# Optimization experiments

Measured on AMD Instinct MI355X. Metric: run time of the kernel, lower is better.

## Reference

```python
import jax, jax.numpy as jnp
import numpy as np

INPUT_DIM = 1024
HIDDEN_DIM = 1024
FORGET_BIAS = 0.0


def setup_inputs() -> dict:
    key = jax.random.key(0)
    ks = jax.random.split(key, 8)
    x = jax.random.normal(ks[0], (1024, 32, INPUT_DIM), dtype=jnp.float32)
    state = jnp.zeros((1, 32, HIDDEN_DIM), dtype=jnp.float32)
    std = 0.1
    wm_z = std * jax.random.normal(ks[1], (HIDDEN_DIM, INPUT_DIM), dtype=jnp.float32)
    wm_f = std * jax.random.normal(ks[2], (HIDDEN_DIM, INPUT_DIM), dtype=jnp.float32)
    wv_z = std * jax.random.normal(ks[3], (1, HIDDEN_DIM), dtype=jnp.float32)
    wv_f = std * jax.random.normal(ks[4], (1, HIDDEN_DIM), dtype=jnp.float32)
    bias_z = std * jax.random.normal(ks[5], (1, HIDDEN_DIM), dtype=jnp.float32)
    bias_f = std * jax.random.normal(ks[6], (1, HIDDEN_DIM), dtype=jnp.float32) + FORGET_BIAS
    return {"x": x, "state": state, "wm_z": wm_z, "wm_f": wm_f,
            "wv_z": wv_z, "wv_f": wv_f, "bias_z": bias_z, "bias_f": bias_f}


def reference(x, state, wm_z, wm_f, wv_z, wv_f, bias_z, bias_f):
    # x: [slen, bsz, in_dim]; state: [1, bsz, hidden]
    hidden_prev = state[0]  # [bsz, hidden]
    # Pre-activation input projections (batched GEMM over all timesteps).
    out_z = jnp.einsum('sbi,hi->sbh', x, wm_z)  # [slen, bsz, hidden]
    out_f = jnp.einsum('sbi,hi->sbh', x, wm_f)

    def step(cell, zf):
        z_, f_ = zf
        z_part = jnp.tanh(z_ + wv_z * cell + bias_z)
        f_part = jax.nn.sigmoid(f_ + wv_f * cell + bias_f)
        new_cell = cell * f_part + (1.0 - f_part) * z_part
        return new_cell, new_cell

    _, new_cells = jax.lax.scan(step, hidden_prev, (out_z, out_f))
    return new_cells  # [slen, bsz, hidden]
```

## Files before the change

kernel.cpp:

```cpp
#include <hip/hip_runtime.h>
#include <hip/hip_fp16.h>

#define S_LEN 1024
#define BSZ   32
#define IN_DIM 1024
#define HID   1024
#define MDIM  (S_LEN*BSZ)
#define NDIM  (2*HID)
#define KDIM  IN_DIM

typedef __attribute__((ext_vector_type(8)))  _Float16 half8;
typedef __attribute__((ext_vector_type(2)))  _Float16 half2v;
typedef __attribute__((ext_vector_type(4)))  float    floatx4;

#define NXV ((MDIM*KDIM)/8)
__global__ void cvt_xw_kernel(const float* __restrict__ x,
                              const float* __restrict__ wz, const float* __restrict__ wf,
                              _Float16* __restrict__ xh, _Float16* __restrict__ wh) {
    int idx = blockIdx.x * blockDim.x + threadIdx.x;
    const float4* s4;
    half8* dst;
    if (idx < NXV) {
        s4 = (const float4*)x + (size_t)idx * 2;
        dst = (half8*)xh + idx;
    } else {
        int wi = idx - NXV;
        int e0 = wi * 8;
        int r   = e0 >> 10;
        int col = e0 & 1023;
        int g = r >> 5, sub = r & 31;
        const float* src = (sub < 16)
            ? wz + ((size_t)(g * 16 + sub)      * KDIM + col)
            : wf + ((size_t)(g * 16 + sub - 16) * KDIM + col);
        s4 = (const float4*)src;
        dst = (half8*)wh + wi;
    }
    float4 a = s4[0], b = s4[1];
    half8 h;
    h[0] = (_Float16)a.x; h[1] = (_Float16)a.y; h[2] = (_Float16)a.z; h[3] = (_Float16)a.w;
    h[4] = (_Float16)b.x; h[5] = (_Float16)b.y; h[6] = (_Float16)b.z; h[7] = (_Float16)b.w;
    *dst = h;
}

#define BM 256
#define BN 256
#define BK 64
#define TPB 4
#define NGT (TPB * 16)
#define NIT (NGT / 2)

__global__ __launch_bounds__(512, 2) void gemm_f16_kernel(
    const _Float16* __restrict__ A, const _Float16* __restrict__ B,
    uint* __restrict__ zf) {
    __shared__ __attribute__((aligned(128))) _Float16 smem[65536];
    char* smb = (char*)smem;

    const int tid  = threadIdx.x;
    const int lane = tid & 63;
    const int wv   = tid >> 6;
    const int wm_off = (wv >> 2) * 128;
    const int wn_off = (wv & 3) * 64;

    const int b      = blockIdx.x;
    const int mchunk = (b & 7) + 8 * ((b >> 3) & 3);
    const int m_bs   = mchunk * (TPB * BM);
    const int n0g    = (b >> 5) * BN;

    const int fr  = lane & 15;
    const int fkb = (lane >> 4) * 16;

    const int srow = lane >> 3;
    const int skb  = ((lane & 7) ^ srow) << 4;

    floatx4 acc[8][4] = {};

    auto STAGE_A = [&](int g, int R0) {
        int kt = g & 15, mt = (g >> 4) & 3;
        int r = R0 + wv * 8 + srow;
        const _Float16* gp = A + (size_t)(m_bs + mt * BM + r) * KDIM + kt * BK + (skb >> 1);
        __builtin_amdgcn_global_load_lds(
            (const __attribute__((address_space(1))) void*)gp,
            (__attribute__((address_space(3))) void*)(smb + (g & 1) * 65536 + (R0 + wv * 8) * 128),
            16, 0, 0);
    };
    auto STAGE_B = [&](int g, int R0) {
        int kt = g & 15;
        int r = R0 + wv * 8 + srow;
        const _Float16* gp = B + (size_t)(n0g + r) * KDIM + kt * BK + (skb >> 1);
        __builtin_amdgcn_global_load_lds(
            (const __attribute__((address_space(1))) void*)gp,
            (__attribute__((address_space(3))) void*)(smb + (g & 1) * 65536 + 32768 + (R0 + wv * 8) * 128),
            16, 0, 0);
    };
    auto LD8 = [&](int rb, int r, int kb) -> half8 {
        return *(const half8*)(smb + rb + r * 128 + (kb ^ ((r & 7) << 4)));
    };

    STAGE_B(0, 0);   STAGE_B(0, 64);
    STAGE_A(0, 0);   STAGE_A(0, 128);
    STAGE_B(0, 128); STAGE_B(0, 192);
    STAGE_A(0, 64);  STAGE_A(0, 192);
    STAGE_B(1, 0);   STAGE_B(1, 64);
    STAGE_A(1, 0);   STAGE_A(1, 128);
    STAGE_B(1, 128); STAGE_B(1, 192);
    asm volatile("s_waitcnt vmcnt(6)" ::: "memory");
    __builtin_amdgcn_s_barrier();
    asm volatile("" ::: "memory");

    half8 bfr[4][2];
    half8 afrA[2][2], afrB[2][2];
    for (int it = 0; it < NIT; ++it) {
        const int  t    = 2 * it;
        const bool more = (it < NIT - 1);
        #pragma unroll
        for (int ph = 0; ph < 8; ++ph) {
            const int q     = ph & 3;
            const int bbase = (ph >> 2) * 65536;

            if (q == 0) {
                #pragma unroll
                for (int j = 0; j < 4; ++j)
                    #pragma unroll
                    for (int ks = 0; ks < 2; ++ks)
                        bfr[j][ks] = LD8(bbase + 32768, wn_off + j * 16 + fr, ks * 64 + fkb);
                #pragma unroll
                for (int ii = 0; ii < 2; ++ii)
                    #pragma unroll
                    for (int ks = 0; ks < 2; ++ks) {
                        afrA[ii][ks] = LD8(bbase, wm_off + ii * 16 + fr,        ks * 64 + fkb);
                        afrB[ii][ks] = LD8(bbase, wm_off + (2 + ii) * 16 + fr,  ks * 64 + fkb);
                    }
            } else if (q == 1) {
                #pragma unroll
                for (int ii = 0; ii < 2; ++ii)
                    #pragma unroll
                    for (int ks = 0; ks < 2; ++ks)
                        afrA[ii][ks] = LD8(bbase, wm_off + (4 + ii) * 16 + fr, ks * 64 + fkb);
            } else if (q == 2) {
                #pragma unroll
                for (int ii = 0; ii < 2; ++ii)
                    #pragma unroll
                    for (int ks = 0; ks < 2; ++ks)
                        afrB[ii][ks] = LD8(bbase, wm_off + (6 + ii) * 16 + fr, ks * 64 + fkb);
            }

            if (ph == 0) {
                STAGE_A(t + 1, 64);  STAGE_A(t + 1, 192);
            } else if (more) {
                if      (ph == 1) { STAGE_B(t + 2, 0);   STAGE_B(t + 2, 64);  }
                else if (ph == 2) { STAGE_A(t + 2, 0);   STAGE_A(t + 2, 128); }
                else if (ph == 3) { STAGE_B(t + 2, 128); STAGE_B(t + 2, 192); }
                else if (ph == 4) { STAGE_A(t + 2, 64);  STAGE_A(t + 2, 192); }
                else if (ph == 5) { STAGE_B(t + 3, 0);   STAGE_B(t + 3, 64);  }
                else if (ph == 6) { STAGE_A(t + 3, 0);   STAGE_A(t + 3, 128); }
                else              { STAGE_B(t + 3, 128); STAGE_B(t + 3, 192); }
            }

            __builtin_amdgcn_s_barrier();
            asm volatile("" ::: "memory");
            __builtin_amdgcn_s_setprio(1);
            if (q == 0 || q == 2) {
                #pragma unroll
                for (int ks = 0; ks < 2; ++ks)
                    #pragma unroll
                    for (int ii = 0; ii < 2; ++ii)
                        #pragma unroll
                        for (int j = 0; j < 4; ++j)
                            acc[2 * q + ii][j] = __builtin_amdgcn_mfma_f32_16x16x32_f16(
                                afrA[ii][ks], bfr[j][ks], acc[2 * q + ii][j], 0, 0, 0);
            } else {
                #pragma unroll
                for (int ks = 0; ks < 2; ++ks)
                    #pragma unroll
                    for (int ii = 0; ii < 2; ++ii)
                        #pragma unroll
                        for (int j = 0; j < 4; ++j)
                            acc[2 * q + ii][j] = __builtin_amdgcn_mfma_f32_16x16x32_f16(
                                afrB[ii][ks], bfr[j][ks], acc[2 * q + ii][j], 0, 0, 0);
            }
            __builtin_amdgcn_s_setprio(0);
            if (ph == 3) {
                if (more) asm volatile("s_waitcnt vmcnt(6)" ::: "memory");
                else      asm volatile("s_waitcnt vmcnt(0)" ::: "memory");
            } else if (ph == 7) {
                if (more) asm volatile("s_waitcnt vmcnt(6)" ::: "memory");
            }
            __builtin_amdgcn_s_barrier();
            asm volatile("" ::: "memory");
        }

        if ((it & 7) == 7) {
            const int m0   = m_bs + (it >> 3) * BM;
            const int orow = (lane >> 4) * 4;
            const int ocol = lane & 15;
            const int gb   = (n0g + wn_off) >> 5;
            #pragma unroll
            for (int i = 0; i < 8; ++i)
                #pragma unroll
                for (int p2 = 0; p2 < 2; ++p2) {
                    int hh = (gb + p2) * 16 + ocol;
                    #pragma unroll
                    for (int r = 0; r < 4; ++r) {
                        int row = m0 + wm_off + i * 16 + orow + r;
                        half2v v;
                        v[0] = (_Float16)acc[i][2 * p2][r];
                        v[1] = (_Float16)acc[i][2 * p2 + 1][r];
                        *(half2v*)(zf + (size_t)row * HID + hh) = v;
                    }
                }
            #pragma unroll
            for (int i = 0; i < 8; ++i)
                #pragma unroll
                for (int j = 0; j < 4; ++j)
                    acc[i][j] = (floatx4)0.0f;
        }
    }
}

#define UNR 32
__device__ __forceinline__ float fast_exp2(float x) {
    float r;
    asm("v_exp_f32 %0, %1" : "=v"(r) : "v"(x));
    return r;
}
__global__ __launch_bounds__(64) void scan_kernel(
    const uint* __restrict__ zf, float* __restrict__ out,
    const float* __restrict__ state,
    const float* __restrict__ wvz, const float* __restrict__ wvf,
    const float* __restrict__ bz, const float* __restrict__ bfv) {
    const int t = blockIdx.x * 64 + threadIdx.x;
    const int h = t & (HID - 1);
    const int stride = BSZ * HID;

    float cell = state[t];
    const float L2E = 1.44269504088896f;
    const float azt = 2.0f * L2E * wvz[h];
    const float czt = 2.0f * L2E * bz[h];
    const float aft = -L2E * wvf[h];
    const float cft = -L2E * bfv[h];

    const uint* p = zf + t;
    float* po = out + t;

    uint buf[UNR];
    #pragma unroll
    for (int u = 0; u < UNR; ++u) buf[u] = p[(size_t)u * stride];

    for (int s0 = 0; s0 < S_LEN; s0 += UNR) {
        uint nb[UNR];
        if (s0 + UNR < S_LEN) {
            #pragma unroll
            for (int u = 0; u < UNR; ++u)
                nb[u] = p[(size_t)(s0 + UNR + u) * stride];
        }
        #pragma unroll
        for (int u = 0; u < UNR; ++u) {
            half2v h2 = __builtin_bit_cast(half2v, buf[u]);
            float zb = fmaf((float)h2[0], 2.0f * L2E, czt);
            float fb = fmaf((float)h2[1], -L2E, cft);
            float ez = fast_exp2(fmaf(azt, cell, zb));
            float zp = fmaf(-2.0f, __builtin_amdgcn_rcpf(ez + 1.0f), 1.0f);
            float ef = fast_exp2(fmaf(aft, cell, fb));
            float fp = __builtin_amdgcn_rcpf(ef + 1.0f);
            cell = fmaf(cell - zp, fp, zp);
            po[(size_t)(s0 + u) * stride] = cell;
        }
        #pragma unroll
        for (int u = 0; u < UNR; ++u) buf[u] = nb[u];
    }
}

extern "C" void kernel_launch(void* const* d_in, const int* in_sizes, int n_in,
                              void* d_out, int out_size, void* d_ws, size_t ws_size,
                              hipStream_t stream) {
    const float* x      = (const float*)d_in[0];
    const float* state  = (const float*)d_in[1];
    const float* wm_z   = (const float*)d_in[2];
    const float* wm_f   = (const float*)d_in[3];
    const float* wv_z   = (const float*)d_in[4];
    const float* wv_f   = (const float*)d_in[5];
    const float* bias_z = (const float*)d_in[6];
    const float* bias_f = (const float*)d_in[7];
    float* out = (float*)d_out;

    char* ws = (char*)d_ws;
    _Float16* xh = (_Float16*)ws;
    _Float16* wh = (_Float16*)(ws + (size_t)MDIM * KDIM * sizeof(_Float16));
    uint* zf     = (uint*)(ws + (size_t)MDIM * KDIM * sizeof(_Float16)
                              + (size_t)NDIM * KDIM * sizeof(_Float16));

    cvt_xw_kernel<<<((MDIM + NDIM) * KDIM) / (256 * 8), 256, 0, stream>>>(
        x, wm_z, wm_f, xh, wh);

    gemm_f16_kernel<<<256, 512, 0, stream>>>(xh, wh, zf);

    scan_kernel<<<MDIM / 64, 64, 0, stream>>>(zf, out, state, wv_z, wv_f, bias_z, bias_f);
}
```

Measured before the change: 430.5 us.

## Simplify A-fragment loads per phase and deepen scan unrolling

The GEMM kernel stops double-buffering A fragments across phases (afrA/afrB) and instead loads only the two fragments needed in each phase, then waits on lgkmcnt before the MFMAs. This cuts register pressure but exposes LDS latency right before compute. The scan kernel's unroll depth is doubled and its launch bounds now state one block per SM. The goal is more memory-level parallelism in the sequential scan loop.

```diff
diff --git a/kernel.cpp b/kernel.cpp
--- a/kernel.cpp
+++ b/kernel.cpp
@@ -108,7 +108,6 @@
     asm volatile("" ::: "memory");
 
     half8 bfr[4][2];
-    half8 afrA[2][2], afrB[2][2];
     for (int it = 0; it < NIT; ++it) {
         const int  t    = 2 * it;
         const bool more = (it < NIT - 1);
@@ -123,26 +122,13 @@
                     #pragma unroll
                     for (int ks = 0; ks < 2; ++ks)
                         bfr[j][ks] = LD8(bbase + 32768, wn_off + j * 16 + fr, ks * 64 + fkb);
-                #pragma unroll
-                for (int ii = 0; ii < 2; ++ii)
-                    #pragma unroll
-                    for (int ks = 0; ks < 2; ++ks) {
-                        afrA[ii][ks] = LD8(bbase, wm_off + ii * 16 + fr,        ks * 64 + fkb);
-                        afrB[ii][ks] = LD8(bbase, wm_off + (2 + ii) * 16 + fr,  ks * 64 + fkb);
-                    }
-            } else if (q == 1) {
-                #pragma unroll
-                for (int ii = 0; ii < 2; ++ii)
-                    #pragma unroll
-                    for (int ks = 0; ks < 2; ++ks)
-                        afrA[ii][ks] = LD8(bbase, wm_off + (4 + ii) * 16 + fr, ks * 64 + fkb);
-            } else if (q == 2) {
-                #pragma unroll
-                for (int ii = 0; ii < 2; ++ii)
-                    #pragma unroll
-                    for (int ks = 0; ks < 2; ++ks)
-                        afrB[ii][ks] = LD8(bbase, wm_off + (6 + ii) * 16 + fr, ks * 64 + fkb);
             }
+            half8 afr[2][2];
+            #pragma unroll
+            for (int ii = 0; ii < 2; ++ii)
+                #pragma unroll
+                for (int ks = 0; ks < 2; ++ks)
+                    afr[ii][ks] = LD8(bbase, wm_off + (2 * q + ii) * 16 + fr, ks * 64 + fkb);
 
             if (ph == 0) {
                 STAGE_A(t + 1, 64);  STAGE_A(t + 1, 192);
@@ -157,27 +143,16 @@
             }
 
             __builtin_amdgcn_s_barrier();
-            asm volatile("" ::: "memory");
+            asm volatile("s_waitcnt lgkmcnt(0)" ::: "memory");
             __builtin_amdgcn_s_setprio(1);
-            if (q == 0 || q == 2) {
-                #pragma unroll
-                for (int ks = 0; ks < 2; ++ks)
+            #pragma unroll
+            for (int ks = 0; ks < 2; ++ks)
+                #pragma unroll
+                for (int ii = 0; ii < 2; ++ii)
                     #pragma unroll
-                    for (int ii = 0; ii < 2; ++ii)
-                        #pragma unroll
-                        for (int j = 0; j < 4; ++j)
-                            acc[2 * q + ii][j] = __builtin_amdgcn_mfma_f32_16x16x32_f16(
-                                afrA[ii][ks], bfr[j][ks], acc[2 * q + ii][j], 0, 0, 0);
-            } else {
-                #pragma unroll
-                for (int ks = 0; ks < 2; ++ks)
-                    #pragma unroll
-                    for (int ii = 0; ii < 2; ++ii)
-                        #pragma unroll
-                        for (int j = 0; j < 4; ++j)
-                            acc[2 * q + ii][j] = __builtin_amdgcn_mfma_f32_16x16x32_f16(
-                                afrB[ii][ks], bfr[j][ks], acc[2 * q + ii][j], 0, 0, 0);
-            }
+                    for (int j = 0; j < 4; ++j)
+                        acc[2 * q + ii][j] = __builtin_amdgcn_mfma_f32_16x16x32_f16(
+                            afr[ii][ks], bfr[j][ks], acc[2 * q + ii][j], 0, 0, 0);
             __builtin_amdgcn_s_setprio(0);
             if (ph == 3) {
                 if (more) asm volatile("s_waitcnt vmcnt(6)" ::: "memory");
@@ -217,13 +192,13 @@
     }
 }
 
-#define UNR 32
+#define UNR 64
 __device__ __forceinline__ float fast_exp2(float x) {
     float r;
     asm("v_exp_f32 %0, %1" : "=v"(r) : "v"(x));
     return r;
 }
-__global__ __launch_bounds__(64) void scan_kernel(
+__global__ __launch_bounds__(64, 1) void scan_kernel(
     const uint* __restrict__ zf, float* __restrict__ out,
     const float* __restrict__ state,
     const float* __restrict__ wvz, const float* __restrict__ wvf,
```

Measured after the change: 412.3 us. 1.04x faster.
